# Optimization experiments

Hardware: AMD Instinct MI355X
Metric: run time of the kernel (lower is better)

The kernel has to match this reference:

```python
import jax, jax.numpy as jnp
import numpy as np

IMAGE_SIZE = 128
PATCH_SIZE = 8
BOND_DIM = 128
CP_RANK = 64
EMBED_DIM = 512
BATCH = 512
GRID = IMAGE_SIZE // PATCH_SIZE            # 16
NUM_PATCHES = GRID * GRID                  # 256
DEPTH = 4                                  # log4(256)
LEVEL_NODES = [64, 16, 4, 1]


def setup_inputs() -> dict:
    key = jax.random.key(0)
    ks = jax.random.split(key, 32)
    s = 0.02
    inp = {
        "x": jax.random.normal(ks[0], (BATCH, 1, IMAGE_SIZE, IMAGE_SIZE), jnp.float32),
        "W_patch": jax.random.normal(ks[1], (PATCH_SIZE * PATCH_SIZE, BOND_DIM), jnp.float32) * s,
        "b_patch": jnp.zeros((BOND_DIM,), jnp.float32),
        "pos": jax.random.normal(ks[2], (1, NUM_PATCHES, BOND_DIM), jnp.float32),
        "gamma": jnp.ones((BOND_DIM,), jnp.float32),
        "beta": jnp.zeros((BOND_DIM,), jnp.float32),
        "W_head": jax.random.normal(ks[3], (BOND_DIM, EMBED_DIM), jnp.float32) * s,
        "b_head": jnp.zeros((EMBED_DIM,), jnp.float32),
    }
    for lvl, n in enumerate(LEVEL_NODES):
        # per-node distinct CP factors: 4 children in_dim->rank, then rank->out_dim
        inp[f"f{lvl}"] = jax.random.normal(ks[4 + 2 * lvl], (n, 4, BOND_DIM, CP_RANK), jnp.float32) * s
        inp[f"o{lvl}"] = jax.random.normal(ks[5 + 2 * lvl], (n, CP_RANK, BOND_DIM), jnp.float32) * s
    return inp


def _patchify(x):
    # 'b c (h p1) (w p2) -> b (h w) (p1 p2 c)', c == 1
    b = x.shape[0]
    x = x.reshape(b, 1, GRID, PATCH_SIZE, GRID, PATCH_SIZE)
    x = x.transpose(0, 2, 4, 3, 5, 1)                  # b h w p1 p2 c
    return x.reshape(b, NUM_PATCHES, PATCH_SIZE * PATCH_SIZE)


def _quad_group(x, grid):
    # 'b (h w) c -> b (h/2 w/2) (h2 w2) c' with 2x2 blocks
    b, _, c = x.shape
    g2 = grid // 2
    x = x.reshape(b, g2, 2, g2, 2, c).transpose(0, 1, 3, 2, 4, 5)
    return x.reshape(b, g2 * g2, 4, c)


def _cp_level(x, f, o):
    # x: [b, n, 4, C]; f: [n, 4, C, R]; o: [n, R, C]
    u = jnp.einsum('bnqc,nqcr->bnqr', x, f)
    p = jnp.prod(u, axis=2)                            # [b, n, R]
    return jnp.einsum('bnr,nrc->bnc', p, o)


def reference(x, W_patch, b_patch, pos, f0, o0, f1, o1, f2, o2, f3, o3,
              gamma, beta, W_head, b_head):
    h = _patchify(x) @ W_patch + b_patch               # [b, 256, C]
    h = h + pos
    grid = GRID
    for f, o in ((f0, o0), (f1, o1), (f2, o2), (f3, o3)):
        h = _cp_level(_quad_group(h, grid), f, o)
        grid //= 2
    h = h[:, 0, :]                                     # squeeze node dim
    mu = jnp.mean(h, axis=-1, keepdims=True)
    var = jnp.var(h, axis=-1, keepdims=True)
    h = (h - mu) / jnp.sqrt(var + 1e-5) * gamma + beta
    out = h @ W_head + b_head
    n = jnp.maximum(jnp.linalg.norm(out, axis=-1, keepdims=True), 1e-12)
    return out / n
```

## Files before the change

kernel.cpp:

```cpp
#include <hip/hip_runtime.h>
#include <hip/hip_bf16.h>

#define BATCH     512
#define IMG       128
#define PS        8
#define GRID_P    16
#define NP        256
#define C         128
#define R         64
#define E         512

typedef float f32x4 __attribute__((ext_vector_type(4)));
typedef short s16x8 __attribute__((ext_vector_type(8)));

__device__ __forceinline__ unsigned short f2bf(float x) {
    unsigned int u = __float_as_uint(x);
    u += 0x7fffu + ((u >> 16) & 1u);
    return (unsigned short)(u >> 16);
}
__device__ __forceinline__ float bf2f(unsigned short h) {
    return __uint_as_float(((unsigned int)h) << 16);
}

__global__ __launch_bounds__(256) void prep_all_kernel(
    const float* __restrict__ f0, const float* __restrict__ f1,
    const float* __restrict__ f2, const float* __restrict__ f3,
    const float* __restrict__ o0, const float* __restrict__ o1,
    const float* __restrict__ o2, const float* __restrict__ o3,
    const float* __restrict__ Wh, const float* __restrict__ Wp,
    const float* __restrict__ pos, const float* __restrict__ bp,
    unsigned short* __restrict__ fTL, unsigned short* __restrict__ oT,
    unsigned short* __restrict__ WhT, unsigned short* __restrict__ WfT,
    float* __restrict__ pf)
{
    __shared__ float ls[128 * 68];
    __shared__ float red[64 * 4];
    const int bi = blockIdx.x, t = threadIdx.x;

    if (bi < 256) {
        const float* src = f0 + (size_t)bi * 8192;
#pragma unroll
        for (int i = 0; i < 8; ++i) {
            const int fi = (t + 256 * i) * 4;
            const int c = fi >> 6, r = fi & 63;
            *(float4*)(ls + c * 68 + r) = *(const float4*)(src + fi);
        }
        __syncthreads();

        const int w = t >> 6, lane = t & 63;
        const int m = lane & 15, g = lane >> 4;

        f32x4 acc[4];
#pragma unroll
        for (int nt = 0; nt < 4; ++nt) acc[nt] = (f32x4){0.f, 0.f, 0.f, 0.f};
#pragma unroll
        for (int kt = 0; kt < 4; ++kt) {
            s16x8 afr;
#pragma unroll
            for (int e = 0; e < 8; ++e)
                afr[e] = (short)f2bf(ls[(kt * 32 + g * 8 + e) * 68 + w * 16 + m]);
#pragma unroll
            for (int nt = 0; nt < 4; ++nt) {
                const float* wr = Wp + (size_t)(nt * 16 + m) * 128 + kt * 32 + g * 8;
                const float4 b0 = *(const float4*)wr;
                const float4 b1 = *(const float4*)(wr + 4);
                s16x8 bfr;
                bfr[0] = (short)f2bf(b0.x); bfr[1] = (short)f2bf(b0.y);
                bfr[2] = (short)f2bf(b0.z); bfr[3] = (short)f2bf(b0.w);
                bfr[4] = (short)f2bf(b1.x); bfr[5] = (short)f2bf(b1.y);
                bfr[6] = (short)f2bf(b1.z); bfr[7] = (short)f2bf(b1.w);
                acc[nt] = __builtin_amdgcn_mfma_f32_16x16x32_bf16(afr, bfr, acc[nt], 0, 0, 0);
            }
        }
        unsigned short* D = WfT + (size_t)bi * 4096;
#pragma unroll
        for (int nt = 0; nt < 4; ++nt)
#pragma unroll
            for (int j = 0; j < 4; ++j)
                D[(size_t)(w * 16 + g * 4 + j) * 64 + nt * 16 + m] = f2bf(acc[nt][j]);

        {
            const int r = t & 63, half = t >> 6;
            const int n0 = bi >> 2, q = bi & 3;
            const int pp = (2 * (n0 >> 3) + (q >> 1)) * GRID_P + 2 * (n0 & 7) + (q & 1);
            const float* posr = pos + (size_t)pp * C;
            float s = 0.f;
#pragma unroll 8
            for (int e = 0; e < 32; ++e) {
                const int c = half * 32 + e;
                s += (posr[c] + bp[c]) * ls[c * 68 + r];
            }
            red[r * 4 + half] = s;
        }
        __syncthreads();
        if (t < 64)
            pf[bi * 64 + t] = red[t * 4 + 0] + red[t * 4 + 1] + red[t * 4 + 2] + red[t * 4 + 3];
    } else if (bi < 340) {
        const int ti = bi - 256;
        const float* src;
        if      (ti < 64) src = f1 + (size_t)ti * 8192;
        else if (ti < 80) src = f2 + (size_t)(ti - 64) * 8192;
        else              src = f3 + (size_t)(ti - 80) * 8192;
        unsigned short* dst = fTL + (size_t)ti * 8192;
#pragma unroll
        for (int i = 0; i < 8; ++i) {
            const int fi = (t + 256 * i) * 4;
            const int c = fi >> 6, r = fi & 63;
            *(float4*)(ls + c * 68 + r) = *(const float4*)(src + fi);
        }
        __syncthreads();
        const int rr = t >> 2, seg = t & 3;
        unsigned int* d32 = (unsigned int*)(dst + rr * 128 + seg * 32);
#pragma unroll
        for (int ii = 0; ii < 16; ++ii) {
            const int c = seg * 32 + ii * 2;
            const unsigned int lo = f2bf(ls[c * 68 + rr]);
            const unsigned int hi = f2bf(ls[(c + 1) * 68 + rr]);
            d32[ii] = lo | (hi << 16);
        }
    } else if (bi < 425) {
        const int oi = bi - 340;
        const float* src;
        if      (oi < 64) src = o0 + (size_t)oi * 8192;
        else if (oi < 80) src = o1 + (size_t)(oi - 64) * 8192;
        else if (oi < 84) src = o2 + (size_t)(oi - 80) * 8192;
        else              src = o3 + (size_t)(oi - 84) * 8192;
        unsigned short* dst = oT + (size_t)oi * 8192;
#pragma unroll
        for (int i = 0; i < 8; ++i) {
            const int fi = (t + 256 * i) * 4;
            const int r = fi >> 7, c = fi & 127;
            *(float4*)(ls + r * 132 + c) = *(const float4*)(src + fi);
        }
        __syncthreads();
        const int cc = t >> 1, seg = t & 1;
        unsigned int* d32 = (unsigned int*)(dst + cc * 64 + seg * 32);
#pragma unroll
        for (int ii = 0; ii < 16; ++ii) {
            const int r = seg * 32 + ii * 2;
            const unsigned int lo = f2bf(ls[r * 132 + cc]);
            const unsigned int hi = f2bf(ls[(r + 1) * 132 + cc]);
            d32[ii] = lo | (hi << 16);
        }
    } else {
        const int j = bi - 425;
#pragma unroll
        for (int i = 0; i < 8; ++i) {
            const int fi = (t + 256 * i) * 4;
            const int c = fi >> 6, e = fi & 63;
            *(float4*)(ls + c * 68 + e) = *(const float4*)(Wh + (size_t)c * E + j * 64 + e);
        }
        __syncthreads();
        const int rr = t >> 2, seg = t & 3;
        unsigned int* d32 = (unsigned int*)(WhT + (size_t)(j * 64 + rr) * 128 + seg * 32);
#pragma unroll
        for (int ii = 0; ii < 16; ++ii) {
            const int c = seg * 32 + ii * 2;
            const unsigned int lo = f2bf(ls[c * 68 + rr]);
            const unsigned int hi = f2bf(ls[(c + 1) * 68 + rr]);
            d32[ii] = lo | (hi << 16);
        }
    }
}

__global__ __launch_bounds__(256) void level01_fused(
    const float* __restrict__ x,
    const unsigned short* __restrict__ WfT,
    const float* __restrict__ pf,
    const unsigned short* __restrict__ oT,
    const unsigned short* __restrict__ fT1,
    unsigned short* __restrict__ h2)
{
    __shared__ __align__(16) unsigned short pixs[16 * 1026];
    __shared__ __align__(16) float          us1[4 * 16 * 68];
    __shared__ __align__(16) unsigned short ps0[4 * 16 * 72];
    __shared__ __align__(16) unsigned short ps1[16 * 72];
    __shared__ __align__(16) unsigned short h1s[4 * 16 * 136];

    const int bi = blockIdx.x;
    const int n1 = bi >> 5, btile = bi & 31;
    const int t = threadIdx.x, w = t >> 6, lane = t & 63;
    const int m = lane & 15, g = lane >> 4;
    const int bt = btile * 16;

    const int y1g = n1 >> 2, x1g = n1 & 3;
    const int Ry0 = y1g * 32, Rx0 = x1g * 32;
    const int n0 = (2 * y1g + (w >> 1)) * 8 + 2 * x1g + (w & 1);

#pragma unroll
    for (int i = 0; i < 16; ++i) {
        const int idx = i * 256 + t;
        const int c4 = idx & 7, rowg = (idx >> 3) & 31, bl = idx >> 8;
        const float4 p4 = *(const float4*)(x + ((size_t)(bt + bl) * IMG + Ry0 + rowg) * IMG + Rx0 + c4 * 4);
        uint2 v;
        v.x = (unsigned int)f2bf(p4.x) | ((unsigned int)f2bf(p4.y) << 16);
        v.y = (unsigned int)f2bf(p4.z) | ((unsigned int)f2bf(p4.w) << 16);
        *(uint2*)(pixs + bl * 1026 + rowg * 32 + c4 * 4) = v;
    }
    __syncthreads();

    s16x8 a[4][2];
    {
        const int rbase = 16 * (w >> 1);
        const int cbase = 16 * (w & 1);
#pragma unroll
        for (int q = 0; q < 4; ++q) {
            const int rq = rbase + 8 * (q >> 1) + g;
            const int cc = cbase + 8 * (q & 1);
#pragma unroll
            for (int kt = 0; kt < 2; ++kt)
                a[q][kt] = *(const s16x8*)(pixs + m * 1026 + (rq + kt * 4) * 32 + cc);
        }
    }

    f32x4 accu[4][4];
#pragma unroll
    for (int q = 0; q < 4; ++q) {
        const float* pfq = pf + (size_t)(n0 * 4 + q) * 64;
#pragma unroll
        for (int nt = 0; nt < 4; ++nt) {
            const float pv = pfq[nt * 16 + m];
            accu[q][nt] = (f32x4){pv, pv, pv, pv};
        }
    }
#pragma unroll
    for (int q = 0; q < 4; ++q) {
        const unsigned short* Wq = WfT + (size_t)(n0 * 4 + q) * 4096;
#pragma unroll
        for (int kt = 0; kt < 2; ++kt) {
            const int koff = kt * 32 + g * 8;
#pragma unroll
            for (int nt = 0; nt < 4; ++nt) {
                const s16x8 bfr = *(const s16x8*)(Wq + (size_t)(nt * 16 + m) * 64 + koff);
                accu[q][nt] = __builtin_amdgcn_mfma_f32_16x16x32_bf16(a[q][kt], bfr, accu[q][nt], 0, 0, 0);
            }
        }
    }

    unsigned short* myps = ps0 + w * (16 * 72);
#pragma unroll
    for (int nt = 0; nt < 4; ++nt) {
        const f32x4 pr = accu[0][nt] * accu[1][nt] * accu[2][nt] * accu[3][nt];
#pragma unroll
        for (int j = 0; j < 4; ++j)
            myps[(g * 4 + j) * 72 + nt * 16 + m] = f2bf(pr[j]);
    }

    {
        s16x8 ap[2];
#pragma unroll
        for (int kt = 0; kt < 2; ++kt)
            ap[kt] = *(const s16x8*)(myps + m * 72 + kt * 32 + g * 8);
        const unsigned short* oTn = oT + (size_t)n0 * 8192;
        unsigned short* myh = h1s + w * (16 * 136);
#pragma unroll
        for (int ct = 0; ct < 8; ++ct) {
            f32x4 aco = (f32x4){0.f, 0.f, 0.f, 0.f};
#pragma unroll
            for (int kt = 0; kt < 2; ++kt) {
                const s16x8 bfr = *(const s16x8*)(oTn + (size_t)(ct * 16 + m) * 64 + kt * 32 + g * 8);
                aco = __builtin_amdgcn_mfma_f32_16x16x32_bf16(ap[kt], bfr, aco, 0, 0, 0);
            }
#pragma unroll
            for (int j = 0; j < 4; ++j)
                myh[(g * 4 + j) * 136 + ct * 16 + m] = f2bf(aco[j]);
        }
    }

    {
        const unsigned short* myh = h1s + w * (16 * 136);
        const unsigned short* fq = fT1 + (size_t)(n1 * 4 + w) * 8192;
        f32x4 au[4];
#pragma unroll
        for (int nt = 0; nt < 4; ++nt) au[nt] = (f32x4){0.f, 0.f, 0.f, 0.f};
#pragma unroll
        for (int kt = 0; kt < 4; ++kt) {
            const int koff = kt * 32 + g * 8;
            const s16x8 afr = *(const s16x8*)(myh + m * 136 + koff);
#pragma unroll
            for (int nt = 0; nt < 4; ++nt) {
                const s16x8 bfr = *(const s16x8*)(fq + (size_t)(nt * 16 + m) * 128 + koff);
                au[nt] = __builtin_amdgcn_mfma_f32_16x16x32_bf16(afr, bfr, au[nt], 0, 0, 0);
            }
        }
#pragma unroll
        for (int nt = 0; nt < 4; ++nt)
#pragma unroll
            for (int j = 0; j < 4; ++j)
                us1[(w * 16 + g * 4 + j) * 68 + nt * 16 + m] = au[nt][j];
    }
    __syncthreads();

    {
        const int pb = t >> 4, r0 = (t & 15) * 4;
        const f32x4 u0 = *(const f32x4*)(us1 + (0 * 16 + pb) * 68 + r0);
        const f32x4 u1 = *(const f32x4*)(us1 + (1 * 16 + pb) * 68 + r0);
        const f32x4 u2 = *(const f32x4*)(us1 + (2 * 16 + pb) * 68 + r0);
        const f32x4 u3 = *(const f32x4*)(us1 + (3 * 16 + pb) * 68 + r0);
        const f32x4 p = u0 * u1 * u2 * u3;
        uint2 v;
        v.x = (unsigned int)f2bf(p[0]) | ((unsigned int)f2bf(p[1]) << 16);
        v.y = (unsigned int)f2bf(p[2]) | ((unsigned int)f2bf(p[3]) << 16);
        *(uint2*)(ps1 + pb * 72 + r0) = v;
    }
    __syncthreads();

    {
        s16x8 ap[2];
#pragma unroll
        for (int kt = 0; kt < 2; ++kt)
            ap[kt] = *(const s16x8*)(ps1 + m * 72 + kt * 32 + g * 8);
        const unsigned short* oTn = oT + (size_t)(64 + n1) * 8192;
#pragma unroll
        for (int i = 0; i < 2; ++i) {
            const int ct = w * 2 + i;
            f32x4 aco = (f32x4){0.f, 0.f, 0.f, 0.f};
#pragma unroll
            for (int kt = 0; kt < 2; ++kt) {
                const s16x8 bfr = *(const s16x8*)(oTn + (size_t)(ct * 16 + m) * 64 + kt * 32 + g * 8);
                aco = __builtin_amdgcn_mfma_f32_16x16x32_bf16(ap[kt], bfr, aco, 0, 0, 0);
            }
#pragma unroll
            for (int j = 0; j < 4; ++j)
                h2[((size_t)(bt + g * 4 + j) * 16 + n1) * C + ct * 16 + m] = f2bf(aco[j]);
        }
    }
}

__global__ __launch_bounds__(256) void tail_kernel(
    const unsigned short* __restrict__ h2,
    const unsigned short* __restrict__ fT2,
    const unsigned short* __restrict__ oT2,
    const unsigned short* __restrict__ fT3,
    const unsigned short* __restrict__ oT3,
    const float* __restrict__ gamma, const float* __restrict__ beta,
    const unsigned short* __restrict__ WhT,
    const float* __restrict__ bh,
    float* __restrict__ out)
{
    __shared__ __align__(16) float          us3[4 * 16 * 68];
    __shared__ __align__(16) unsigned short ps2[4 * 16 * 72];
    __shared__ __align__(16) unsigned short ps3[16 * 72];
    __shared__ __align__(16) unsigned short h3s[16 * 4 * 136];
    __shared__ __align__(16) float          h4s[16 * 132];
    __shared__ __align__(16) unsigned short hns[16 * 136];
    __shared__ float red[16 * 4];

    const int bt = blockIdx.x * 16;
    const int t = threadIdx.x, w = t >> 6, lane = t & 63;
    const int m = lane & 15, g = lane >> 4;

    {
        const int n2 = w;
        const int y1 = n2 >> 1, x1 = n2 & 1;
        f32x4 acc_u[4][4];
#pragma unroll
        for (int q = 0; q < 4; ++q)
#pragma unroll
            for (int nt = 0; nt < 4; ++nt) acc_u[q][nt] = (f32x4){0.f, 0.f, 0.f, 0.f};
#pragma unroll
        for (int q = 0; q < 4; ++q) {
            const int pidx = (2 * y1 + (q >> 1)) * 4 + 2 * x1 + (q & 1);
            const unsigned short* xq = h2 + ((size_t)(bt + m) * 16 + pidx) * C;
            const unsigned short* fq = fT2 + (size_t)(n2 * 4 + q) * R * C;
#pragma unroll
            for (int kt = 0; kt < 4; ++kt) {
                const int koff = kt * 32 + g * 8;
                const s16x8 a = *(const s16x8*)(xq + koff);
#pragma unroll
                for (int nt = 0; nt < 4; ++nt) {
                    const s16x8 bfr = *(const s16x8*)(fq + (size_t)(nt * 16 + m) * C + koff);
                    acc_u[q][nt] = __builtin_amdgcn_mfma_f32_16x16x32_bf16(a, bfr, acc_u[q][nt], 0, 0, 0);
                }
            }
        }
        unsigned short* myps = ps2 + w * 16 * 72;
#pragma unroll
        for (int nt = 0; nt < 4; ++nt) {
            const f32x4 p = acc_u[0][nt] * acc_u[1][nt] * acc_u[2][nt] * acc_u[3][nt];
#pragma unroll
            for (int j = 0; j < 4; ++j)
                myps[(g * 4 + j) * 72 + nt * 16 + m] = f2bf(p[j]);
        }
        f32x4 aco[8];
#pragma unroll
        for (int ct = 0; ct < 8; ++ct) aco[ct] = (f32x4){0.f, 0.f, 0.f, 0.f};
        const unsigned short* oTn = oT2 + (size_t)n2 * C * R;
#pragma unroll
        for (int kt = 0; kt < 2; ++kt) {
            const int koff = kt * 32 + g * 8;
            const s16x8 a = *(const s16x8*)(myps + m * 72 + koff);
#pragma unroll
            for (int ct = 0; ct < 8; ++ct) {
                const s16x8 bfr = *(const s16x8*)(oTn + (size_t)(ct * 16 + m) * R + koff);
                aco[ct] = __builtin_amdgcn_mfma_f32_16x16x32_bf16(a, bfr, aco[ct], 0, 0, 0);
            }
        }
#pragma unroll
        for (int ct = 0; ct < 8; ++ct)
#pragma unroll
            for (int j = 0; j < 4; ++j)
                h3s[((g * 4 + j) * 4 + n2) * 136 + ct * 16 + m] = f2bf(aco[ct][j]);
    }
    __syncthreads();

    {
        const int q = w;
        const unsigned short* fq = fT3 + (size_t)q * R * C;
        f32x4 acc_u[4];
#pragma unroll
        for (int nt = 0; nt < 4; ++nt) acc_u[nt] = (f32x4){0.f, 0.f, 0.f, 0.f};
#pragma unroll
        for (int kt = 0; kt < 4; ++kt) {
            const int koff = kt * 32 + g * 8;
            const s16x8 a = *(const s16x8*)(h3s + (m * 4 + q) * 136 + koff);
#pragma unroll
            for (int nt = 0; nt < 4; ++nt) {
                const s16x8 bfr = *(const s16x8*)(fq + (size_t)(nt * 16 + m) * C + koff);
                acc_u[nt] = __builtin_amdgcn_mfma_f32_16x16x32_bf16(a, bfr, acc_u[nt], 0, 0, 0);
            }
        }
#pragma unroll
        for (int nt = 0; nt < 4; ++nt)
#pragma unroll
            for (int j = 0; j < 4; ++j)
                us3[(q * 16 + g * 4 + j) * 68 + nt * 16 + m] = acc_u[nt][j];
    }
    __syncthreads();
    {
        const int pb = t >> 4, r0 = (t & 15) * 4;
        const f32x4 u0 = *(const f32x4*)(us3 + (0 * 16 + pb) * 68 + r0);
        const f32x4 u1 = *(const f32x4*)(us3 + (1 * 16 + pb) * 68 + r0);
        const f32x4 u2 = *(const f32x4*)(us3 + (2 * 16 + pb) * 68 + r0);
        const f32x4 u3 = *(const f32x4*)(us3 + (3 * 16 + pb) * 68 + r0);
        const f32x4 p = u0 * u1 * u2 * u3;
        uint2 v;
        v.x = (unsigned int)f2bf(p[0]) | ((unsigned int)f2bf(p[1]) << 16);
        v.y = (unsigned int)f2bf(p[2]) | ((unsigned int)f2bf(p[3]) << 16);
        *(uint2*)(ps3 + pb * 72 + r0) = v;
    }
    __syncthreads();
    {
        s16x8 ap[2];
#pragma unroll
        for (int kt = 0; kt < 2; ++kt)
            ap[kt] = *(const s16x8*)(ps3 + m * 72 + kt * 32 + g * 8);
#pragma unroll
        for (int i = 0; i < 2; ++i) {
            f32x4 aco = (f32x4){0.f, 0.f, 0.f, 0.f};
            const int ct = w * 2 + i;
#pragma unroll
            for (int kt = 0; kt < 2; ++kt) {
                const s16x8 bfr = *(const s16x8*)(oT3 + (size_t)(ct * 16 + m) * R + kt * 32 + g * 8);
                aco = __builtin_amdgcn_mfma_f32_16x16x32_bf16(ap[kt], bfr, aco, 0, 0, 0);
            }
#pragma unroll
            for (int j = 0; j < 4; ++j)
                h4s[(g * 4 + j) * 132 + ct * 16 + m] = aco[j];
        }
    }
    __syncthreads();

    {
        const int rb = w * 4 + g;
        const int c0 = m * 8;
        const f32x4 v0 = *(const f32x4*)(h4s + rb * 132 + c0);
        const f32x4 v1 = *(const f32x4*)(h4s + rb * 132 + c0 + 4);
        float s  = v0[0] + v0[1] + v0[2] + v0[3] + v1[0] + v1[1] + v1[2] + v1[3];
        float ss = v0[0]*v0[0] + v0[1]*v0[1] + v0[2]*v0[2] + v0[3]*v0[3]
                 + v1[0]*v1[0] + v1[1]*v1[1] + v1[2]*v1[2] + v1[3]*v1[3];
#pragma unroll
        for (int off = 1; off < 16; off <<= 1) {
            s  += __shfl_xor(s, off);
            ss += __shfl_xor(ss, off);
        }
        const float mu   = s * (1.f / C);
        const float var  = ss * (1.f / C) - mu * mu;
        const float rstd = rsqrtf(var + 1e-5f);
        const f32x4 ga0 = *(const f32x4*)(gamma + c0);
        const f32x4 ga1 = *(const f32x4*)(gamma + c0 + 4);
        const f32x4 be0 = *(const f32x4*)(beta + c0);
        const f32x4 be1 = *(const f32x4*)(beta + c0 + 4);
        unsigned int o32[4];
        float hv[8];
#pragma unroll
        for (int k = 0; k < 4; ++k) hv[k]     = (v0[k] - mu) * rstd * ga0[k] + be0[k];
#pragma unroll
        for (int k = 0; k < 4; ++k) hv[4 + k] = (v1[k] - mu) * rstd * ga1[k] + be1[k];
#pragma unroll
        for (int k = 0; k < 4; ++k)
            o32[k] = (unsigned int)f2bf(hv[2*k]) | ((unsigned int)f2bf(hv[2*k+1]) << 16);
        *(uint4*)(hns + rb * 136 + c0) = *(uint4*)o32;
    }
    __syncthreads();

    {
        f32x4 acc[8];
#pragma unroll
        for (int nt = 0; nt < 8; ++nt) {
            const int e = w * 128 + nt * 16 + m;
            const float bv = bh[e];
            acc[nt] = (f32x4){bv, bv, bv, bv};
        }
#pragma unroll
        for (int kt = 0; kt < 4; ++kt) {
            const int koff = kt * 32 + g * 8;
            const s16x8 a = *(const s16x8*)(hns + m * 136 + koff);
#pragma unroll
            for (int nt = 0; nt < 8; ++nt) {
                const int e = w * 128 + nt * 16 + m;
                const s16x8 bfr = *(const s16x8*)(WhT + (size_t)e * 128 + koff);
                acc[nt] = __builtin_amdgcn_mfma_f32_16x16x32_bf16(a, bfr, acc[nt], 0, 0, 0);
            }
        }
        float sq[4];
#pragma unroll
        for (int j = 0; j < 4; ++j) {
            float s = 0.f;
#pragma unroll
            for (int nt = 0; nt < 8; ++nt) s += acc[nt][j] * acc[nt][j];
#pragma unroll
            for (int off = 1; off < 16; off <<= 1) s += __shfl_xor(s, off);
            sq[j] = s;
        }
        if (m == 0) {
#pragma unroll
            for (int j = 0; j < 4; ++j) red[(g * 4 + j) * 4 + w] = sq[j];
        }
        __syncthreads();
#pragma unroll
        for (int j = 0; j < 4; ++j) {
            const int row = g * 4 + j;
            const float tot = red[row * 4 + 0] + red[row * 4 + 1]
                            + red[row * 4 + 2] + red[row * 4 + 3];
            const float inv = 1.f / fmaxf(sqrtf(tot), 1e-12f);
#pragma unroll
            for (int nt = 0; nt < 8; ++nt) {
                const int e = w * 128 + nt * 16 + m;
                out[(size_t)(bt + row) * E + e] = acc[nt][j] * inv;
            }
        }
    }
}

extern "C" void kernel_launch(void* const* d_in, const int* in_sizes, int n_in,
                              void* d_out, int out_size, void* d_ws, size_t ws_size,
                              hipStream_t stream) {
    const float* x     = (const float*)d_in[0];
    const float* Wp    = (const float*)d_in[1];
    const float* bp    = (const float*)d_in[2];
    const float* pos   = (const float*)d_in[3];
    const float* gamma = (const float*)d_in[4];
    const float* beta  = (const float*)d_in[5];
    const float* Wh    = (const float*)d_in[6];
    const float* bh    = (const float*)d_in[7];
    const float* f0    = (const float*)d_in[8];
    const float* o0    = (const float*)d_in[9];
    const float* f1    = (const float*)d_in[10];
    const float* o1    = (const float*)d_in[11];
    const float* f2    = (const float*)d_in[12];
    const float* o2    = (const float*)d_in[13];
    const float* f3    = (const float*)d_in[14];
    const float* o3    = (const float*)d_in[15];
    float* out = (float*)d_out;

    unsigned short* h2  = (unsigned short*)d_ws;
    unsigned short* fTL = h2 + (size_t)1048576;
    unsigned short* oT  = fTL + (size_t)688128;
    unsigned short* WfT = oT + (size_t)696320;
    unsigned short* WhT = WfT + (size_t)1048576;
    float*          pff = (float*)(WhT + 65536);

    unsigned short* fT1 = fTL;
    unsigned short* fT2 = fTL + (size_t)64 * 8192;
    unsigned short* fT3 = fTL + (size_t)80 * 8192;
    unsigned short* oT2 = oT + (size_t)80 * 8192;
    unsigned short* oT3 = oT + (size_t)84 * 8192;

    prep_all_kernel<<<433, 256, 0, stream>>>(f0, f1, f2, f3, o0, o1, o2, o3,
                                             Wh, Wp, pos, bp,
                                             fTL, oT, WhT, WfT, pff);

    level01_fused<<<16 * 32, 256, 0, stream>>>(x, WfT, pff, oT, fT1, h2);

    tail_kernel<<<32, 256, 0, stream>>>(h2, fT2, oT2, fT3, oT3,
                                        gamma, beta, WhT, bh, out);
}
```

Baseline: 152.5 us.

## Fuse prep, level01 and tail kernels into one cooperative mega-kernel

```diff
diff --git a/kernel.cpp b/kernel.cpp
--- a/kernel.cpp
+++ b/kernel.cpp
@@ -1,5 +1,8 @@
 #include <hip/hip_runtime.h>
 #include <hip/hip_bf16.h>
+#include <hip/hip_cooperative_groups.h>
+
+namespace cg = cooperative_groups;
 
 #define BATCH     512
 #define IMG       128
@@ -22,522 +25,514 @@
     return __uint_as_float(((unsigned int)h) << 16);
 }
 
-__global__ __launch_bounds__(256) void prep_all_kernel(
-    const float* __restrict__ f0, const float* __restrict__ f1,
-    const float* __restrict__ f2, const float* __restrict__ f3,
-    const float* __restrict__ o0, const float* __restrict__ o1,
-    const float* __restrict__ o2, const float* __restrict__ o3,
-    const float* __restrict__ Wh, const float* __restrict__ Wp,
-    const float* __restrict__ pos, const float* __restrict__ bp,
+__global__ __launch_bounds__(256) void ttn_mega_kernel(
+    const float* __restrict__ x,  const float* __restrict__ Wp,
+    const float* __restrict__ bp, const float* __restrict__ pos,
+    const float* __restrict__ gamma, const float* __restrict__ beta,
+    const float* __restrict__ Wh, const float* __restrict__ bh,
+    const float* __restrict__ f0, const float* __restrict__ o0,
+    const float* __restrict__ f1, const float* __restrict__ o1,
+    const float* __restrict__ f2, const float* __restrict__ o2,
+    const float* __restrict__ f3, const float* __restrict__ o3,
     unsigned short* __restrict__ fTL, unsigned short* __restrict__ oT,
     unsigned short* __restrict__ WhT, unsigned short* __restrict__ WfT,
-    float* __restrict__ pf)
-{
-    __shared__ float ls[128 * 68];
-    __shared__ float red[64 * 4];
-    const int bi = blockIdx.x, t = threadIdx.x;
-
-    if (bi < 256) {
-        const float* src = f0 + (size_t)bi * 8192;
-#pragma unroll
-        for (int i = 0; i < 8; ++i) {
-            const int fi = (t + 256 * i) * 4;
-            const int c = fi >> 6, r = fi & 63;
-            *(float4*)(ls + c * 68 + r) = *(const float4*)(src + fi);
-        }
-        __syncthreads();
-
-        const int w = t >> 6, lane = t & 63;
-        const int m = lane & 15, g = lane >> 4;
-
-        f32x4 acc[4];
-#pragma unroll
-        for (int nt = 0; nt < 4; ++nt) acc[nt] = (f32x4){0.f, 0.f, 0.f, 0.f};
-#pragma unroll
-        for (int kt = 0; kt < 4; ++kt) {
-            s16x8 afr;
-#pragma unroll
-            for (int e = 0; e < 8; ++e)
-                afr[e] = (short)f2bf(ls[(kt * 32 + g * 8 + e) * 68 + w * 16 + m]);
-#pragma unroll
-            for (int nt = 0; nt < 4; ++nt) {
-                const float* wr = Wp + (size_t)(nt * 16 + m) * 128 + kt * 32 + g * 8;
-                const float4 b0 = *(const float4*)wr;
-                const float4 b1 = *(const float4*)(wr + 4);
-                s16x8 bfr;
-                bfr[0] = (short)f2bf(b0.x); bfr[1] = (short)f2bf(b0.y);
-                bfr[2] = (short)f2bf(b0.z); bfr[3] = (short)f2bf(b0.w);
-                bfr[4] = (short)f2bf(b1.x); bfr[5] = (short)f2bf(b1.y);
-                bfr[6] = (short)f2bf(b1.z); bfr[7] = (short)f2bf(b1.w);
-                acc[nt] = __builtin_amdgcn_mfma_f32_16x16x32_bf16(afr, bfr, acc[nt], 0, 0, 0);
-            }
-        }
-        unsigned short* D = WfT + (size_t)bi * 4096;
-#pragma unroll
-        for (int nt = 0; nt < 4; ++nt)
-#pragma unroll
-            for (int j = 0; j < 4; ++j)
-                D[(size_t)(w * 16 + g * 4 + j) * 64 + nt * 16 + m] = f2bf(acc[nt][j]);
-
-        {
-            const int r = t & 63, half = t >> 6;
-            const int n0 = bi >> 2, q = bi & 3;
-            const int pp = (2 * (n0 >> 3) + (q >> 1)) * GRID_P + 2 * (n0 & 7) + (q & 1);
-            const float* posr = pos + (size_t)pp * C;
-            float s = 0.f;
-#pragma unroll 8
-            for (int e = 0; e < 32; ++e) {
-                const int c = half * 32 + e;
-                s += (posr[c] + bp[c]) * ls[c * 68 + r];
-            }
-            red[r * 4 + half] = s;
-        }
-        __syncthreads();
-        if (t < 64)
-            pf[bi * 64 + t] = red[t * 4 + 0] + red[t * 4 + 1] + red[t * 4 + 2] + red[t * 4 + 3];
-    } else if (bi < 340) {
-        const int ti = bi - 256;
-        const float* src;
-        if      (ti < 64) src = f1 + (size_t)ti * 8192;
-        else if (ti < 80) src = f2 + (size_t)(ti - 64) * 8192;
-        else              src = f3 + (size_t)(ti - 80) * 8192;
-        unsigned short* dst = fTL + (size_t)ti * 8192;
-#pragma unroll
-        for (int i = 0; i < 8; ++i) {
-            const int fi = (t + 256 * i) * 4;
-            const int c = fi >> 6, r = fi & 63;
-            *(float4*)(ls + c * 68 + r) = *(const float4*)(src + fi);
-        }
-        __syncthreads();
-        const int rr = t >> 2, seg = t & 3;
-        unsigned int* d32 = (unsigned int*)(dst + rr * 128 + seg * 32);
-#pragma unroll
-        for (int ii = 0; ii < 16; ++ii) {
-            const int c = seg * 32 + ii * 2;
-            const unsigned int lo = f2bf(ls[c * 68 + rr]);
-            const unsigned int hi = f2bf(ls[(c + 1) * 68 + rr]);
-            d32[ii] = lo | (hi << 16);
-        }
-    } else if (bi < 425) {
-        const int oi = bi - 340;
-        const float* src;
-        if      (oi < 64) src = o0 + (size_t)oi * 8192;
-        else if (oi < 80) src = o1 + (size_t)(oi - 64) * 8192;
-        else if (oi < 84) src = o2 + (size_t)(oi - 80) * 8192;
-        else              src = o3 + (size_t)(oi - 84) * 8192;
-        unsigned short* dst = oT + (size_t)oi * 8192;
-#pragma unroll
-        for (int i = 0; i < 8; ++i) {
-            const int fi = (t + 256 * i) * 4;
-            const int r = fi >> 7, c = fi & 127;
-            *(float4*)(ls + r * 132 + c) = *(const float4*)(src + fi);
-        }
-        __syncthreads();
-        const int cc = t >> 1, seg = t & 1;
-        unsigned int* d32 = (unsigned int*)(dst + cc * 64 + seg * 32);
-#pragma unroll
-        for (int ii = 0; ii < 16; ++ii) {
-            const int r = seg * 32 + ii * 2;
-            const unsigned int lo = f2bf(ls[r * 132 + cc]);
-            const unsigned int hi = f2bf(ls[(r + 1) * 132 + cc]);
-            d32[ii] = lo | (hi << 16);
-        }
-    } else {
-        const int j = bi - 425;
-#pragma unroll
-        for (int i = 0; i < 8; ++i) {
-            const int fi = (t + 256 * i) * 4;
-            const int c = fi >> 6, e = fi & 63;
-            *(float4*)(ls + c * 68 + e) = *(const float4*)(Wh + (size_t)c * E + j * 64 + e);
-        }
-        __syncthreads();
-        const int rr = t >> 2, seg = t & 3;
-        unsigned int* d32 = (unsigned int*)(WhT + (size_t)(j * 64 + rr) * 128 + seg * 32);
-#pragma unroll
-        for (int ii = 0; ii < 16; ++ii) {
-            const int c = seg * 32 + ii * 2;
-            const unsigned int lo = f2bf(ls[c * 68 + rr]);
-            const unsigned int hi = f2bf(ls[(c + 1) * 68 + rr]);
-            d32[ii] = lo | (hi << 16);
-        }
-    }
-}
-
-__global__ __launch_bounds__(256) void level01_fused(
-    const float* __restrict__ x,
-    const unsigned short* __restrict__ WfT,
-    const float* __restrict__ pf,
-    const unsigned short* __restrict__ oT,
-    const unsigned short* __restrict__ fT1,
-    unsigned short* __restrict__ h2)
-{
-    __shared__ __align__(16) unsigned short pixs[16 * 1026];
-    __shared__ __align__(16) float          us1[4 * 16 * 68];
-    __shared__ __align__(16) unsigned short ps0[4 * 16 * 72];
-    __shared__ __align__(16) unsigned short ps1[16 * 72];
-    __shared__ __align__(16) unsigned short h1s[4 * 16 * 136];
-
-    const int bi = blockIdx.x;
-    const int n1 = bi >> 5, btile = bi & 31;
-    const int t = threadIdx.x, w = t >> 6, lane = t & 63;
-    const int m = lane & 15, g = lane >> 4;
-    const int bt = btile * 16;
-
-    const int y1g = n1 >> 2, x1g = n1 & 3;
-    const int Ry0 = y1g * 32, Rx0 = x1g * 32;
-    const int n0 = (2 * y1g + (w >> 1)) * 8 + 2 * x1g + (w & 1);
-
-#pragma unroll
-    for (int i = 0; i < 16; ++i) {
-        const int idx = i * 256 + t;
-        const int c4 = idx & 7, rowg = (idx >> 3) & 31, bl = idx >> 8;
-        const float4 p4 = *(const float4*)(x + ((size_t)(bt + bl) * IMG + Ry0 + rowg) * IMG + Rx0 + c4 * 4);
-        uint2 v;
-        v.x = (unsigned int)f2bf(p4.x) | ((unsigned int)f2bf(p4.y) << 16);
-        v.y = (unsigned int)f2bf(p4.z) | ((unsigned int)f2bf(p4.w) << 16);
-        *(uint2*)(pixs + bl * 1026 + rowg * 32 + c4 * 4) = v;
-    }
-    __syncthreads();
-
-    s16x8 a[4][2];
-    {
-        const int rbase = 16 * (w >> 1);
-        const int cbase = 16 * (w & 1);
-#pragma unroll
-        for (int q = 0; q < 4; ++q) {
-            const int rq = rbase + 8 * (q >> 1) + g;
-            const int cc = cbase + 8 * (q & 1);
-#pragma unroll
-            for (int kt = 0; kt < 2; ++kt)
-                a[q][kt] = *(const s16x8*)(pixs + m * 1026 + (rq + kt * 4) * 32 + cc);
-        }
-    }
-
-    f32x4 accu[4][4];
-#pragma unroll
-    for (int q = 0; q < 4; ++q) {
-        const float* pfq = pf + (size_t)(n0 * 4 + q) * 64;
-#pragma unroll
-        for (int nt = 0; nt < 4; ++nt) {
-            const float pv = pfq[nt * 16 + m];
-            accu[q][nt] = (f32x4){pv, pv, pv, pv};
-        }
-    }
-#pragma unroll
-    for (int q = 0; q < 4; ++q) {
-        const unsigned short* Wq = WfT + (size_t)(n0 * 4 + q) * 4096;
-#pragma unroll
-        for (int kt = 0; kt < 2; ++kt) {
-            const int koff = kt * 32 + g * 8;
-#pragma unroll
-            for (int nt = 0; nt < 4; ++nt) {
-                const s16x8 bfr = *(const s16x8*)(Wq + (size_t)(nt * 16 + m) * 64 + koff);
-                accu[q][nt] = __builtin_amdgcn_mfma_f32_16x16x32_bf16(a[q][kt], bfr, accu[q][nt], 0, 0, 0);
-            }
-        }
-    }
-
-    unsigned short* myps = ps0 + w * (16 * 72);
-#pragma unroll
-    for (int nt = 0; nt < 4; ++nt) {
-        const f32x4 pr = accu[0][nt] * accu[1][nt] * accu[2][nt] * accu[3][nt];
-#pragma unroll
-        for (int j = 0; j < 4; ++j)
-            myps[(g * 4 + j) * 72 + nt * 16 + m] = f2bf(pr[j]);
-    }
-
-    {
-        s16x8 ap[2];
-#pragma unroll
-        for (int kt = 0; kt < 2; ++kt)
-            ap[kt] = *(const s16x8*)(myps + m * 72 + kt * 32 + g * 8);
-        const unsigned short* oTn = oT + (size_t)n0 * 8192;
-        unsigned short* myh = h1s + w * (16 * 136);
-#pragma unroll
-        for (int ct = 0; ct < 8; ++ct) {
-            f32x4 aco = (f32x4){0.f, 0.f, 0.f, 0.f};
-#pragma unroll
-            for (int kt = 0; kt < 2; ++kt) {
-                const s16x8 bfr = *(const s16x8*)(oTn + (size_t)(ct * 16 + m) * 64 + kt * 32 + g * 8);
-                aco = __builtin_amdgcn_mfma_f32_16x16x32_bf16(ap[kt], bfr, aco, 0, 0, 0);
-            }
-#pragma unroll
-            for (int j = 0; j < 4; ++j)
-                myh[(g * 4 + j) * 136 + ct * 16 + m] = f2bf(aco[j]);
-        }
-    }
-
-    {
-        const unsigned short* myh = h1s + w * (16 * 136);
-        const unsigned short* fq = fT1 + (size_t)(n1 * 4 + w) * 8192;
-        f32x4 au[4];
-#pragma unroll
-        for (int nt = 0; nt < 4; ++nt) au[nt] = (f32x4){0.f, 0.f, 0.f, 0.f};
-#pragma unroll
-        for (int kt = 0; kt < 4; ++kt) {
-            const int koff = kt * 32 + g * 8;
-            const s16x8 afr = *(const s16x8*)(myh + m * 136 + koff);
-#pragma unroll
-            for (int nt = 0; nt < 4; ++nt) {
-                const s16x8 bfr = *(const s16x8*)(fq + (size_t)(nt * 16 + m) * 128 + koff);
-                au[nt] = __builtin_amdgcn_mfma_f32_16x16x32_bf16(afr, bfr, au[nt], 0, 0, 0);
-            }
-        }
-#pragma unroll
-        for (int nt = 0; nt < 4; ++nt)
-#pragma unroll
-            for (int j = 0; j < 4; ++j)
-                us1[(w * 16 + g * 4 + j) * 68 + nt * 16 + m] = au[nt][j];
-    }
-    __syncthreads();
-
-    {
-        const int pb = t >> 4, r0 = (t & 15) * 4;
-        const f32x4 u0 = *(const f32x4*)(us1 + (0 * 16 + pb) * 68 + r0);
-        const f32x4 u1 = *(const f32x4*)(us1 + (1 * 16 + pb) * 68 + r0);
-        const f32x4 u2 = *(const f32x4*)(us1 + (2 * 16 + pb) * 68 + r0);
-        const f32x4 u3 = *(const f32x4*)(us1 + (3 * 16 + pb) * 68 + r0);
-        const f32x4 p = u0 * u1 * u2 * u3;
-        uint2 v;
-        v.x = (unsigned int)f2bf(p[0]) | ((unsigned int)f2bf(p[1]) << 16);
-        v.y = (unsigned int)f2bf(p[2]) | ((unsigned int)f2bf(p[3]) << 16);
-        *(uint2*)(ps1 + pb * 72 + r0) = v;
-    }
-    __syncthreads();
-
-    {
-        s16x8 ap[2];
-#pragma unroll
-        for (int kt = 0; kt < 2; ++kt)
-            ap[kt] = *(const s16x8*)(ps1 + m * 72 + kt * 32 + g * 8);
-        const unsigned short* oTn = oT + (size_t)(64 + n1) * 8192;
-#pragma unroll
-        for (int i = 0; i < 2; ++i) {
-            const int ct = w * 2 + i;
-            f32x4 aco = (f32x4){0.f, 0.f, 0.f, 0.f};
-#pragma unroll
-            for (int kt = 0; kt < 2; ++kt) {
-                const s16x8 bfr = *(const s16x8*)(oTn + (size_t)(ct * 16 + m) * 64 + kt * 32 + g * 8);
-                aco = __builtin_amdgcn_mfma_f32_16x16x32_bf16(ap[kt], bfr, aco, 0, 0, 0);
-            }
-#pragma unroll
-            for (int j = 0; j < 4; ++j)
-                h2[((size_t)(bt + g * 4 + j) * 16 + n1) * C + ct * 16 + m] = f2bf(aco[j]);
-        }
-    }
-}
-
-__global__ __launch_bounds__(256) void tail_kernel(
-    const unsigned short* __restrict__ h2,
-    const unsigned short* __restrict__ fT2,
-    const unsigned short* __restrict__ oT2,
-    const unsigned short* __restrict__ fT3,
-    const unsigned short* __restrict__ oT3,
-    const float* __restrict__ gamma, const float* __restrict__ beta,
-    const unsigned short* __restrict__ WhT,
-    const float* __restrict__ bh,
+    float* __restrict__ pf, unsigned short* __restrict__ h2,
     float* __restrict__ out)
 {
-    __shared__ __align__(16) float          us3[4 * 16 * 68];
-    __shared__ __align__(16) unsigned short ps2[4 * 16 * 72];
-    __shared__ __align__(16) unsigned short ps3[16 * 72];
-    __shared__ __align__(16) unsigned short h3s[16 * 4 * 136];
-    __shared__ __align__(16) float          h4s[16 * 132];
-    __shared__ __align__(16) unsigned short hns[16 * 136];
-    __shared__ float red[16 * 4];
-
-    const int bt = blockIdx.x * 16;
-    const int t = threadIdx.x, w = t >> 6, lane = t & 63;
+    __shared__ __align__(16) char smem[46336];
+    cg::grid_group grid = cg::this_grid();
+
+    const int bi = blockIdx.x, t = threadIdx.x;
+    const int w = t >> 6, lane = t & 63;
     const int m = lane & 15, g = lane >> 4;
 
+    if (bi < 433) {
+        float* ls  = (float*)smem;
+        float* red = (float*)(smem + 34816);
+
+        if (bi < 256) {
+            const float* src = f0 + (size_t)bi * 8192;
+#pragma unroll
+            for (int i = 0; i < 8; ++i) {
+                const int fi = (t + 256 * i) * 4;
+                const int c = fi >> 6, r = fi & 63;
+                *(float4*)(ls + c * 68 + r) = *(const float4*)(src + fi);
+            }
+            __syncthreads();
+
+            f32x4 acc[4];
+#pragma unroll
+            for (int nt = 0; nt < 4; ++nt) acc[nt] = (f32x4){0.f, 0.f, 0.f, 0.f};
+#pragma unroll
+            for (int kt = 0; kt < 4; ++kt) {
+                s16x8 afr;
+#pragma unroll
+                for (int e = 0; e < 8; ++e)
+                    afr[e] = (short)f2bf(ls[(kt * 32 + g * 8 + e) * 68 + w * 16 + m]);
+#pragma unroll
+                for (int nt = 0; nt < 4; ++nt) {
+                    const float* wr = Wp + (size_t)(nt * 16 + m) * 128 + kt * 32 + g * 8;
+                    const float4 b0 = *(const float4*)wr;
+                    const float4 b1 = *(const float4*)(wr + 4);
+                    s16x8 bfr;
+                    bfr[0] = (short)f2bf(b0.x); bfr[1] = (short)f2bf(b0.y);
+                    bfr[2] = (short)f2bf(b0.z); bfr[3] = (short)f2bf(b0.w);
+                    bfr[4] = (short)f2bf(b1.x); bfr[5] = (short)f2bf(b1.y);
+                    bfr[6] = (short)f2bf(b1.z); bfr[7] = (short)f2bf(b1.w);
+                    acc[nt] = __builtin_amdgcn_mfma_f32_16x16x32_bf16(afr, bfr, acc[nt], 0, 0, 0);
+                }
+            }
+            unsigned short* D = WfT + (size_t)bi * 4096;
+#pragma unroll
+            for (int nt = 0; nt < 4; ++nt)
+#pragma unroll
+                for (int j = 0; j < 4; ++j)
+                    D[(size_t)(w * 16 + g * 4 + j) * 64 + nt * 16 + m] = f2bf(acc[nt][j]);
+
+            {
+                const int r = t & 63, half = t >> 6;
+                const int n0 = bi >> 2, q = bi & 3;
+                const int pp = (2 * (n0 >> 3) + (q >> 1)) * GRID_P + 2 * (n0 & 7) + (q & 1);
+                const float* posr = pos + (size_t)pp * C;
+                float s = 0.f;
+#pragma unroll 8
+                for (int e = 0; e < 32; ++e) {
+                    const int c = half * 32 + e;
+                    s += (posr[c] + bp[c]) * ls[c * 68 + r];
+                }
+                red[r * 4 + half] = s;
+            }
+            __syncthreads();
+            if (t < 64)
+                pf[bi * 64 + t] = red[t * 4 + 0] + red[t * 4 + 1] + red[t * 4 + 2] + red[t * 4 + 3];
+        } else if (bi < 340) {
+            const int ti = bi - 256;
+            const float* src;
+            if      (ti < 64) src = f1 + (size_t)ti * 8192;
+            else if (ti < 80) src = f2 + (size_t)(ti - 64) * 8192;
+            else              src = f3 + (size_t)(ti - 80) * 8192;
+            unsigned short* dst = fTL + (size_t)ti * 8192;
+#pragma unroll
+            for (int i = 0; i < 8; ++i) {
+                const int fi = (t + 256 * i) * 4;
+                const int c = fi >> 6, r = fi & 63;
+                *(float4*)(ls + c * 68 + r) = *(const float4*)(src + fi);
+            }
+            __syncthreads();
+            const int rr = t >> 2, seg = t & 3;
+            unsigned int* d32 = (unsigned int*)(dst + rr * 128 + seg * 32);
+#pragma unroll
+            for (int ii = 0; ii < 16; ++ii) {
+                const int c = seg * 32 + ii * 2;
+                const unsigned int lo = f2bf(ls[c * 68 + rr]);
+                const unsigned int hi = f2bf(ls[(c + 1) * 68 + rr]);
+                d32[ii] = lo | (hi << 16);
+            }
+        } else if (bi < 425) {
+            const int oi = bi - 340;
+            const float* src;
+            if      (oi < 64) src = o0 + (size_t)oi * 8192;
+            else if (oi < 80) src = o1 + (size_t)(oi - 64) * 8192;
+            else if (oi < 84) src = o2 + (size_t)(oi - 80) * 8192;
+            else              src = o3 + (size_t)(oi - 84) * 8192;
+            unsigned short* dst = oT + (size_t)oi * 8192;
+#pragma unroll
+            for (int i = 0; i < 8; ++i) {
+                const int fi = (t + 256 * i) * 4;
+                const int r = fi >> 7, c = fi & 127;
+                *(float4*)(ls + r * 132 + c) = *(const float4*)(src + fi);
+            }
+            __syncthreads();
+            const int cc = t >> 1, seg = t & 1;
+            unsigned int* d32 = (unsigned int*)(dst + cc * 64 + seg * 32);
+#pragma unroll
+            for (int ii = 0; ii < 16; ++ii) {
+                const int r = seg * 32 + ii * 2;
+                const unsigned int lo = f2bf(ls[r * 132 + cc]);
+                const unsigned int hi = f2bf(ls[(r + 1) * 132 + cc]);
+                d32[ii] = lo | (hi << 16);
+            }
+        } else {
+            const int j = bi - 425;
+#pragma unroll
+            for (int i = 0; i < 8; ++i) {
+                const int fi = (t + 256 * i) * 4;
+                const int c = fi >> 6, e = fi & 63;
+                *(float4*)(ls + c * 68 + e) = *(const float4*)(Wh + (size_t)c * E + j * 64 + e);
+            }
+            __syncthreads();
+            const int rr = t >> 2, seg = t & 3;
+            unsigned int* d32 = (unsigned int*)(WhT + (size_t)(j * 64 + rr) * 128 + seg * 32);
+#pragma unroll
+            for (int ii = 0; ii < 16; ++ii) {
+                const int c = seg * 32 + ii * 2;
+                const unsigned int lo = f2bf(ls[c * 68 + rr]);
+                const unsigned int hi = f2bf(ls[(c + 1) * 68 + rr]);
+                d32[ii] = lo | (hi << 16);
+            }
+        }
+    }
+    grid.sync();
+
     {
-        const int n2 = w;
-        const int y1 = n2 >> 1, x1 = n2 & 1;
-        f32x4 acc_u[4][4];
-#pragma unroll
-        for (int q = 0; q < 4; ++q)
-#pragma unroll
-            for (int nt = 0; nt < 4; ++nt) acc_u[q][nt] = (f32x4){0.f, 0.f, 0.f, 0.f};
+        unsigned short* pixs = (unsigned short*)smem;
+        float*          us1  = (float*)smem;
+        unsigned short* ps0  = (unsigned short*)(smem + 17408);
+        unsigned short* ps1  = (unsigned short*)(smem + 26624);
+        unsigned short* h1s  = (unsigned short*)(smem + 28928);
+
+        const int n1 = bi >> 5, btile = bi & 31;
+        const int bt = btile * 16;
+        const int y1g = n1 >> 2, x1g = n1 & 3;
+        const int Ry0 = y1g * 32, Rx0 = x1g * 32;
+        const int n0 = (2 * y1g + (w >> 1)) * 8 + 2 * x1g + (w & 1);
+
+#pragma unroll
+        for (int i = 0; i < 16; ++i) {
+            const int idx = i * 256 + t;
+            const int c4 = idx & 7, rowg = (idx >> 3) & 31, bl = idx >> 8;
+            const float4 p4 = *(const float4*)(x + ((size_t)(bt + bl) * IMG + Ry0 + rowg) * IMG + Rx0 + c4 * 4);
+            uint2 v;
+            v.x = (unsigned int)f2bf(p4.x) | ((unsigned int)f2bf(p4.y) << 16);
+            v.y = (unsigned int)f2bf(p4.z) | ((unsigned int)f2bf(p4.w) << 16);
+            *(uint2*)(pixs + bl * 1026 + rowg * 32 + c4 * 4) = v;
+        }
+        __syncthreads();
+
+        s16x8 a[4][2];
+        {
+            const int rbase = 16 * (w >> 1);
+            const int cbase = 16 * (w & 1);
+#pragma unroll
+            for (int q = 0; q < 4; ++q) {
+                const int rq = rbase + 8 * (q >> 1) + g;
+                const int cc = cbase + 8 * (q & 1);
+#pragma unroll
+                for (int kt = 0; kt < 2; ++kt)
+                    a[q][kt] = *(const s16x8*)(pixs + m * 1026 + (rq + kt * 4) * 32 + cc);
+            }
+        }
+        __syncthreads();
+
+        f32x4 accu[4][4];
 #pragma unroll
         for (int q = 0; q < 4; ++q) {
-            const int pidx = (2 * y1 + (q >> 1)) * 4 + 2 * x1 + (q & 1);
-            const unsigned short* xq = h2 + ((size_t)(bt + m) * 16 + pidx) * C;
-            const unsigned short* fq = fT2 + (size_t)(n2 * 4 + q) * R * C;
+            const float* pfq = pf + (size_t)(n0 * 4 + q) * 64;
+#pragma unroll
+            for (int nt = 0; nt < 4; ++nt) {
+                const float pv = pfq[nt * 16 + m];
+                accu[q][nt] = (f32x4){pv, pv, pv, pv};
+            }
+        }
+#pragma unroll
+        for (int q = 0; q < 4; ++q) {
+            const unsigned short* Wq = WfT + (size_t)(n0 * 4 + q) * 4096;
+#pragma unroll
+            for (int kt = 0; kt < 2; ++kt) {
+                const int koff = kt * 32 + g * 8;
+#pragma unroll
+                for (int nt = 0; nt < 4; ++nt) {
+                    const s16x8 bfr = *(const s16x8*)(Wq + (size_t)(nt * 16 + m) * 64 + koff);
+                    accu[q][nt] = __builtin_amdgcn_mfma_f32_16x16x32_bf16(a[q][kt], bfr, accu[q][nt], 0, 0, 0);
+                }
+            }
+        }
+
+        unsigned short* myps = ps0 + w * (16 * 72);
+#pragma unroll
+        for (int nt = 0; nt < 4; ++nt) {
+            const f32x4 pr = accu[0][nt] * accu[1][nt] * accu[2][nt] * accu[3][nt];
+#pragma unroll
+            for (int j = 0; j < 4; ++j)
+                myps[(g * 4 + j) * 72 + nt * 16 + m] = f2bf(pr[j]);
+        }
+
+        {
+            s16x8 ap[2];
+#pragma unroll
+            for (int kt = 0; kt < 2; ++kt)
+                ap[kt] = *(const s16x8*)(myps + m * 72 + kt * 32 + g * 8);
+            const unsigned short* oTn = oT + (size_t)n0 * 8192;
+            unsigned short* myh = h1s + w * (16 * 136);
+#pragma unroll
+            for (int ct = 0; ct < 8; ++ct) {
+                f32x4 aco = (f32x4){0.f, 0.f, 0.f, 0.f};
+#pragma unroll
+                for (int kt = 0; kt < 2; ++kt) {
+                    const s16x8 bfr = *(const s16x8*)(oTn + (size_t)(ct * 16 + m) * 64 + kt * 32 + g * 8);
+                    aco = __builtin_amdgcn_mfma_f32_16x16x32_bf16(ap[kt], bfr, aco, 0, 0, 0);
+                }
+#pragma unroll
+                for (int j = 0; j < 4; ++j)
+                    myh[(g * 4 + j) * 136 + ct * 16 + m] = f2bf(aco[j]);
+            }
+        }
+
+        {
+            const unsigned short* myh = h1s + w * (16 * 136);
+            const unsigned short* fq = fTL + (size_t)(n1 * 4 + w) * 8192;
+            f32x4 au[4];
+#pragma unroll
+            for (int nt = 0; nt < 4; ++nt) au[nt] = (f32x4){0.f, 0.f, 0.f, 0.f};
 #pragma unroll
             for (int kt = 0; kt < 4; ++kt) {
                 const int koff = kt * 32 + g * 8;
-                const s16x8 a = *(const s16x8*)(xq + koff);
+                const s16x8 afr = *(const s16x8*)(myh + m * 136 + koff);
+#pragma unroll
+                for (int nt = 0; nt < 4; ++nt) {
+                    const s16x8 bfr = *(const s16x8*)(fq + (size_t)(nt * 16 + m) * 128 + koff);
+                    au[nt] = __builtin_amdgcn_mfma_f32_16x16x32_bf16(afr, bfr, au[nt], 0, 0, 0);
+                }
+            }
+#pragma unroll
+            for (int nt = 0; nt < 4; ++nt)
+#pragma unroll
+                for (int j = 0; j < 4; ++j)
+                    us1[(w * 16 + g * 4 + j) * 68 + nt * 16 + m] = au[nt][j];
+        }
+        __syncthreads();
+
+        {
+            const int pb = t >> 4, r0 = (t & 15) * 4;
+            const f32x4 u0 = *(const f32x4*)(us1 + (0 * 16 + pb) * 68 + r0);
+            const f32x4 u1 = *(const f32x4*)(us1 + (1 * 16 + pb) * 68 + r0);
+            const f32x4 u2 = *(const f32x4*)(us1 + (2 * 16 + pb) * 68 + r0);
+            const f32x4 u3 = *(const f32x4*)(us1 + (3 * 16 + pb) * 68 + r0);
+            const f32x4 p = u0 * u1 * u2 * u3;
+            uint2 v;
+            v.x = (unsigned int)f2bf(p[0]) | ((unsigned int)f2bf(p[1]) << 16);
+            v.y = (unsigned int)f2bf(p[2]) | ((unsigned int)f2bf(p[3]) << 16);
+            *(uint2*)(ps1 + pb * 72 + r0) = v;
+        }
+        __syncthreads();
+
+        {
+            s16x8 ap[2];
+#pragma unroll
+            for (int kt = 0; kt < 2; ++kt)
+                ap[kt] = *(const s16x8*)(ps1 + m * 72 + kt * 32 + g * 8);
+            const unsigned short* oTn = oT + (size_t)(64 + n1) * 8192;
+#pragma unroll
+            for (int i = 0; i < 2; ++i) {
+                const int ct = w * 2 + i;
+                f32x4 aco = (f32x4){0.f, 0.f, 0.f, 0.f};
+#pragma unroll
+                for (int kt = 0; kt < 2; ++kt) {
+                    const s16x8 bfr = *(const s16x8*)(oTn + (size_t)(ct * 16 + m) * 64 + kt * 32 + g * 8);
+                    aco = __builtin_amdgcn_mfma_f32_16x16x32_bf16(ap[kt], bfr, aco, 0, 0, 0);
+                }
+#pragma unroll
+                for (int j = 0; j < 4; ++j)
+                    h2[((size_t)(bt + g * 4 + j) * 16 + n1) * C + ct * 16 + m] = f2bf(aco[j]);
+            }
+        }
+    }
+    grid.sync();
+
+    if (bi < 32) {
+        float*          us3 = (float*)smem;
+        float*          h4s = (float*)smem;
+        unsigned short* hns = (unsigned short*)(smem + 8448);
+        float*          red = (float*)(smem + 12800);
+        unsigned short* ps2 = (unsigned short*)(smem + 17408);
+        unsigned short* ps3 = (unsigned short*)(smem + 26624);
+        unsigned short* h3s = (unsigned short*)(smem + 28928);
+
+        const int bt = bi * 16;
+        const unsigned short* fT2 = fTL + (size_t)64 * 8192;
+        const unsigned short* fT3 = fTL + (size_t)80 * 8192;
+        const unsigned short* oT2 = oT + (size_t)80 * 8192;
+        const unsigned short* oT3 = oT + (size_t)84 * 8192;
+
+        {
+            const int n2 = w;
+            const int y1 = n2 >> 1, x1 = n2 & 1;
+            f32x4 acc_u[4][4];
+#pragma unroll
+            for (int q = 0; q < 4; ++q)
+#pragma unroll
+                for (int nt = 0; nt < 4; ++nt) acc_u[q][nt] = (f32x4){0.f, 0.f, 0.f, 0.f};
+#pragma unroll
+            for (int q = 0; q < 4; ++q) {
+                const int pidx = (2 * y1 + (q >> 1)) * 4 + 2 * x1 + (q & 1);
+                const unsigned short* xq = h2 + ((size_t)(bt + m) * 16 + pidx) * C;
+                const unsigned short* fq = fT2 + (size_t)(n2 * 4 + q) * R * C;
+#pragma unroll
+                for (int kt = 0; kt < 4; ++kt) {
+                    const int koff = kt * 32 + g * 8;
+                    const s16x8 afr = *(const s16x8*)(xq + koff);
+#pragma unroll
+                    for (int nt = 0; nt < 4; ++nt) {
+                        const s16x8 bfr = *(const s16x8*)(fq + (size_t)(nt * 16 + m) * C + koff);
+                        acc_u[q][nt] = __builtin_amdgcn_mfma_f32_16x16x32_bf16(afr, bfr, acc_u[q][nt], 0, 0, 0);
+                    }
+                }
+            }
+            unsigned short* myps = ps2 + w * 16 * 72;
+#pragma unroll
+            for (int nt = 0; nt < 4; ++nt) {
+                const f32x4 p = acc_u[0][nt] * acc_u[1][nt] * acc_u[2][nt] * acc_u[3][nt];
+#pragma unroll
+                for (int j = 0; j < 4; ++j)
+                    myps[(g * 4 + j) * 72 + nt * 16 + m] = f2bf(p[j]);
+            }
+            f32x4 aco[8];
+#pragma unroll
+            for (int ct = 0; ct < 8; ++ct) aco[ct] = (f32x4){0.f, 0.f, 0.f, 0.f};
+            const unsigned short* oTn = oT2 + (size_t)n2 * C * R;
+#pragma unroll
+            for (int kt = 0; kt < 2; ++kt) {
+                const int koff = kt * 32 + g * 8;
+                const s16x8 afr = *(const s16x8*)(myps + m * 72 + koff);
+#pragma unroll
+                for (int ct = 0; ct < 8; ++ct) {
+                    const s16x8 bfr = *(const s16x8*)(oTn + (size_t)(ct * 16 + m) * R + koff);
+                    aco[ct] = __builtin_amdgcn_mfma_f32_16x16x32_bf16(afr, bfr, aco[ct], 0, 0, 0);
+                }
+            }
+#pragma unroll
+            for (int ct = 0; ct < 8; ++ct)
+#pragma unroll
+                for (int j = 0; j < 4; ++j)
+                    h3s[((g * 4 + j) * 4 + n2) * 136 + ct * 16 + m] = f2bf(aco[ct][j]);
+        }
+        __syncthreads();
+
+        {
+            const int q = w;
+            const unsigned short* fq = fT3 + (size_t)q * R * C;
+            f32x4 acc_u[4];
+#pragma unroll
+            for (int nt = 0; nt < 4; ++nt) acc_u[nt] = (f32x4){0.f, 0.f, 0.f, 0.f};
+#pragma unroll
+            for (int kt = 0; kt < 4; ++kt) {
+                const int koff = kt * 32 + g * 8;
+                const s16x8 afr = *(const s16x8*)(h3s + (m * 4 + q) * 136 + koff);
 #pragma unroll
                 for (int nt = 0; nt < 4; ++nt) {
                     const s16x8 bfr = *(const s16x8*)(fq + (size_t)(nt * 16 + m) * C + koff);
-                    acc_u[q][nt] = __builtin_amdgcn_mfma_f32_16x16x32_bf16(a, bfr, acc_u[q][nt], 0, 0, 0);
-                }
-            }
-        }
-        unsigned short* myps = ps2 + w * 16 * 72;
-#pragma unroll
-        for (int nt = 0; nt < 4; ++nt) {
-            const f32x4 p = acc_u[0][nt] * acc_u[1][nt] * acc_u[2][nt] * acc_u[3][nt];
-#pragma unroll
-            for (int j = 0; j < 4; ++j)
-                myps[(g * 4 + j) * 72 + nt * 16 + m] = f2bf(p[j]);
-        }
-        f32x4 aco[8];
-#pragma unroll
-        for (int ct = 0; ct < 8; ++ct) aco[ct] = (f32x4){0.f, 0.f, 0.f, 0.f};
-        const unsigned short* oTn = oT2 + (size_t)n2 * C * R;
-#pragma unroll
-        for (int kt = 0; kt < 2; ++kt) {
-            const int koff = kt * 32 + g * 8;
-            const s16x8 a = *(const s16x8*)(myps + m * 72 + koff);
-#pragma unroll
-            for (int ct = 0; ct < 8; ++ct) {
-                const s16x8 bfr = *(const s16x8*)(oTn + (size_t)(ct * 16 + m) * R + koff);
-                aco[ct] = __builtin_amdgcn_mfma_f32_16x16x32_bf16(a, bfr, aco[ct], 0, 0, 0);
-            }
-        }
-#pragma unroll
-        for (int ct = 0; ct < 8; ++ct)
-#pragma unroll
-            for (int j = 0; j < 4; ++j)
-                h3s[((g * 4 + j) * 4 + n2) * 136 + ct * 16 + m] = f2bf(aco[ct][j]);
-    }
-    __syncthreads();
-
-    {
-        const int q = w;
-        const unsigned short* fq = fT3 + (size_t)q * R * C;
-        f32x4 acc_u[4];
-#pragma unroll
-        for (int nt = 0; nt < 4; ++nt) acc_u[nt] = (f32x4){0.f, 0.f, 0.f, 0.f};
-#pragma unroll
-        for (int kt = 0; kt < 4; ++kt) {
-            const int koff = kt * 32 + g * 8;
-            const s16x8 a = *(const s16x8*)(h3s + (m * 4 + q) * 136 + koff);
-#pragma unroll
-            for (int nt = 0; nt < 4; ++nt) {
-                const s16x8 bfr = *(const s16x8*)(fq + (size_t)(nt * 16 + m) * C + koff);
-                acc_u[nt] = __builtin_amdgcn_mfma_f32_16x16x32_bf16(a, bfr, acc_u[nt], 0, 0, 0);
-            }
-        }
-#pragma unroll
-        for (int nt = 0; nt < 4; ++nt)
-#pragma unroll
-            for (int j = 0; j < 4; ++j)
-                us3[(q * 16 + g * 4 + j) * 68 + nt * 16 + m] = acc_u[nt][j];
-    }
-    __syncthreads();
-    {
-        const int pb = t >> 4, r0 = (t & 15) * 4;
-        const f32x4 u0 = *(const f32x4*)(us3 + (0 * 16 + pb) * 68 + r0);
-        const f32x4 u1 = *(const f32x4*)(us3 + (1 * 16 + pb) * 68 + r0);
-        const f32x4 u2 = *(const f32x4*)(us3 + (2 * 16 + pb) * 68 + r0);
-        const f32x4 u3 = *(const f32x4*)(us3 + (3 * 16 + pb) * 68 + r0);
-        const f32x4 p = u0 * u1 * u2 * u3;
-        uint2 v;
-        v.x = (unsigned int)f2bf(p[0]) | ((unsigned int)f2bf(p[1]) << 16);
-        v.y = (unsigned int)f2bf(p[2]) | ((unsigned int)f2bf(p[3]) << 16);
-        *(uint2*)(ps3 + pb * 72 + r0) = v;
-    }
-    __syncthreads();
-    {
-        s16x8 ap[2];
-#pragma unroll
-        for (int kt = 0; kt < 2; ++kt)
-            ap[kt] = *(const s16x8*)(ps3 + m * 72 + kt * 32 + g * 8);
-#pragma unroll
-        for (int i = 0; i < 2; ++i) {
-            f32x4 aco = (f32x4){0.f, 0.f, 0.f, 0.f};
-            const int ct = w * 2 + i;
-#pragma unroll
-            for (int kt = 0; kt < 2; ++kt) {
-                const s16x8 bfr = *(const s16x8*)(oT3 + (size_t)(ct * 16 + m) * R + kt * 32 + g * 8);
-                aco = __builtin_amdgcn_mfma_f32_16x16x32_bf16(ap[kt], bfr, aco, 0, 0, 0);
-            }
-#pragma unroll
-            for (int j = 0; j < 4; ++j)
-                h4s[(g * 4 + j) * 132 + ct * 16 + m] = aco[j];
-        }
-    }
-    __syncthreads();
-
-    {
-        const int rb = w * 4 + g;
-        const int c0 = m * 8;
-        const f32x4 v0 = *(const f32x4*)(h4s + rb * 132 + c0);
-        const f32x4 v1 = *(const f32x4*)(h4s + rb * 132 + c0 + 4);
-        float s  = v0[0] + v0[1] + v0[2] + v0[3] + v1[0] + v1[1] + v1[2] + v1[3];
-        float ss = v0[0]*v0[0] + v0[1]*v0[1] + v0[2]*v0[2] + v0[3]*v0[3]
-                 + v1[0]*v1[0] + v1[1]*v1[1] + v1[2]*v1[2] + v1[3]*v1[3];
-#pragma unroll
-        for (int off = 1; off < 16; off <<= 1) {
-            s  += __shfl_xor(s, off);
-            ss += __shfl_xor(ss, off);
-        }
-        const float mu   = s * (1.f / C);
-        const float var  = ss * (1.f / C) - mu * mu;
-        const float rstd = rsqrtf(var + 1e-5f);
-        const f32x4 ga0 = *(const f32x4*)(gamma + c0);
-        const f32x4 ga1 = *(const f32x4*)(gamma + c0 + 4);
-        const f32x4 be0 = *(const f32x4*)(beta + c0);
-        const f32x4 be1 = *(const f32x4*)(beta + c0 + 4);
-        unsigned int o32[4];
-        float hv[8];
-#pragma unroll
-        for (int k = 0; k < 4; ++k) hv[k]     = (v0[k] - mu) * rstd * ga0[k] + be0[k];
-#pragma unroll
-        for (int k = 0; k < 4; ++k) hv[4 + k] = (v1[k] - mu) * rstd * ga1[k] + be1[k];
-#pragma unroll
-        for (int k = 0; k < 4; ++k)
-            o32[k] = (unsigned int)f2bf(hv[2*k]) | ((unsigned int)f2bf(hv[2*k+1]) << 16);
-        *(uint4*)(hns + rb * 136 + c0) = *(uint4*)o32;
-    }
-    __syncthreads();
-
-    {
-        f32x4 acc[8];
-#pragma unroll
-        for (int nt = 0; nt < 8; ++nt) {
-            const int e = w * 128 + nt * 16 + m;
-            const float bv = bh[e];
-            acc[nt] = (f32x4){bv, bv, bv, bv};
-        }
-#pragma unroll
-        for (int kt = 0; kt < 4; ++kt) {
-            const int koff = kt * 32 + g * 8;
-            const s16x8 a = *(const s16x8*)(hns + m * 136 + koff);
+                    acc_u[nt] = __builtin_amdgcn_mfma_f32_16x16x32_bf16(afr, bfr, acc_u[nt], 0, 0, 0);
+                }
+            }
+#pragma unroll
+            for (int nt = 0; nt < 4; ++nt)
+#pragma unroll
+                for (int j = 0; j < 4; ++j)
+                    us3[(q * 16 + g * 4 + j) * 68 + nt * 16 + m] = acc_u[nt][j];
+        }
+        __syncthreads();
+        {
+            const int pb = t >> 4, r0 = (t & 15) * 4;
+            const f32x4 u0 = *(const f32x4*)(us3 + (0 * 16 + pb) * 68 + r0);
+            const f32x4 u1 = *(const f32x4*)(us3 + (1 * 16 + pb) * 68 + r0);
+            const f32x4 u2 = *(const f32x4*)(us3 + (2 * 16 + pb) * 68 + r0);
+            const f32x4 u3 = *(const f32x4*)(us3 + (3 * 16 + pb) * 68 + r0);
+            const f32x4 p = u0 * u1 * u2 * u3;
+            uint2 v;
+            v.x = (unsigned int)f2bf(p[0]) | ((unsigned int)f2bf(p[1]) << 16);
+            v.y = (unsigned int)f2bf(p[2]) | ((unsigned int)f2bf(p[3]) << 16);
+            *(uint2*)(ps3 + pb * 72 + r0) = v;
+        }
+        __syncthreads();
+        {
+            s16x8 ap[2];
+#pragma unroll
+            for (int kt = 0; kt < 2; ++kt)
+                ap[kt] = *(const s16x8*)(ps3 + m * 72 + kt * 32 + g * 8);
+#pragma unroll
+            for (int i = 0; i < 2; ++i) {
+                f32x4 aco = (f32x4){0.f, 0.f, 0.f, 0.f};
+                const int ct = w * 2 + i;
+#pragma unroll
+                for (int kt = 0; kt < 2; ++kt) {
+                    const s16x8 bfr = *(const s16x8*)(oT3 + (size_t)(ct * 16 + m) * R + kt * 32 + g * 8);
+                    aco = __builtin_amdgcn_mfma_f32_16x16x32_bf16(ap[kt], bfr, aco, 0, 0, 0);
+                }
+#pragma unroll
+                for (int j = 0; j < 4; ++j)
+                    h4s[(g * 4 + j) * 132 + ct * 16 + m] = aco[j];
+            }
+        }
+        __syncthreads();
+
+        {
+            const int rb = w * 4 + g;
+            const int c0 = m * 8;
+            const f32x4 v0 = *(const f32x4*)(h4s + rb * 132 + c0);
+            const f32x4 v1 = *(const f32x4*)(h4s + rb * 132 + c0 + 4);
+            float s  = v0[0] + v0[1] + v0[2] + v0[3] + v1[0] + v1[1] + v1[2] + v1[3];
+            float ss = v0[0]*v0[0] + v0[1]*v0[1] + v0[2]*v0[2] + v0[3]*v0[3]
+                     + v1[0]*v1[0] + v1[1]*v1[1] + v1[2]*v1[2] + v1[3]*v1[3];
+#pragma unroll
+            for (int off = 1; off < 16; off <<= 1) {
+                s  += __shfl_xor(s, off);
+                ss += __shfl_xor(ss, off);
+            }
+            const float mu   = s * (1.f / C);
+            const float var  = ss * (1.f / C) - mu * mu;
+            const float rstd = rsqrtf(var + 1e-5f);
+            const f32x4 ga0 = *(const f32x4*)(gamma + c0);
+            const f32x4 ga1 = *(const f32x4*)(gamma + c0 + 4);
+            const f32x4 be0 = *(const f32x4*)(beta + c0);
+            const f32x4 be1 = *(const f32x4*)(beta + c0 + 4);
+            unsigned int o32[4];
+            float hv[8];
+#pragma unroll
+            for (int k = 0; k < 4; ++k) hv[k]     = (v0[k] - mu) * rstd * ga0[k] + be0[k];
+#pragma unroll
+            for (int k = 0; k < 4; ++k) hv[4 + k] = (v1[k] - mu) * rstd * ga1[k] + be1[k];
+#pragma unroll
+            for (int k = 0; k < 4; ++k)
+                o32[k] = (unsigned int)f2bf(hv[2*k]) | ((unsigned int)f2bf(hv[2*k+1]) << 16);
+            *(uint4*)(hns + rb * 136 + c0) = *(uint4*)o32;
+        }
+        __syncthreads();
+
+        {
+            f32x4 acc[8];
 #pragma unroll
             for (int nt = 0; nt < 8; ++nt) {
                 const int e = w * 128 + nt * 16 + m;
-                const s16x8 bfr = *(const s16x8*)(WhT + (size_t)e * 128 + koff);
-                acc[nt] = __builtin_amdgcn_mfma_f32_16x16x32_bf16(a, bfr, acc[nt], 0, 0, 0);
-            }
-        }
-        float sq[4];
-#pragma unroll
-        for (int j = 0; j < 4; ++j) {
-            float s = 0.f;
-#pragma unroll
-            for (int nt = 0; nt < 8; ++nt) s += acc[nt][j] * acc[nt][j];
-#pragma unroll
-            for (int off = 1; off < 16; off <<= 1) s += __shfl_xor(s, off);
-            sq[j] = s;
-        }
-        if (m == 0) {
-#pragma unroll
-            for (int j = 0; j < 4; ++j) red[(g * 4 + j) * 4 + w] = sq[j];
-        }
-        __syncthreads();
-#pragma unroll
-        for (int j = 0; j < 4; ++j) {
-            const int row = g * 4 + j;
-            const float tot = red[row * 4 + 0] + red[row * 4 + 1]
-                            + red[row * 4 + 2] + red[row * 4 + 3];
-            const float inv = 1.f / fmaxf(sqrtf(tot), 1e-12f);
-#pragma unroll
-            for (int nt = 0; nt < 8; ++nt) {
-                const int e = w * 128 + nt * 16 + m;
-                out[(size_t)(bt + row) * E + e] = acc[nt][j] * inv;
+                const float bv = bh[e];
+                acc[nt] = (f32x4){bv, bv, bv, bv};
+            }
+#pragma unroll
+            for (int kt = 0; kt < 4; ++kt) {
+                const int koff = kt * 32 + g * 8;
+                const s16x8 afr = *(const s16x8*)(hns + m * 136 + koff);
+#pragma unroll
+                for (int nt = 0; nt < 8; ++nt) {
+                    const int e = w * 128 + nt * 16 + m;
+                    const s16x8 bfr = *(const s16x8*)(WhT + (size_t)e * 128 + koff);
+                    acc[nt] = __builtin_amdgcn_mfma_f32_16x16x32_bf16(afr, bfr, acc[nt], 0, 0, 0);
+                }
+            }
+            float sq[4];
+#pragma unroll
+            for (int j = 0; j < 4; ++j) {
+                float s = 0.f;
+#pragma unroll
+                for (int nt = 0; nt < 8; ++nt) s += acc[nt][j] * acc[nt][j];
+#pragma unroll
+                for (int off = 1; off < 16; off <<= 1) s += __shfl_xor(s, off);
+                sq[j] = s;
+            }
+            if (m == 0) {
+#pragma unroll
+                for (int j = 0; j < 4; ++j) red[(g * 4 + j) * 4 + w] = sq[j];
+            }
+            __syncthreads();
+#pragma unroll
+            for (int j = 0; j < 4; ++j) {
+                const int row = g * 4 + j;
+                const float tot = red[row * 4 + 0] + red[row * 4 + 1]
+                                + red[row * 4 + 2] + red[row * 4 + 3];
+                const float inv = 1.f / fmaxf(sqrtf(tot), 1e-12f);
+#pragma unroll
+                for (int nt = 0; nt < 8; ++nt) {
+                    const int e = w * 128 + nt * 16 + m;
+                    out[(size_t)(bt + row) * E + e] = acc[nt][j] * inv;
+                }
             }
         }
     }
@@ -571,18 +566,14 @@
     unsigned short* WhT = WfT + (size_t)1048576;
     float*          pff = (float*)(WhT + 65536);
 
-    unsigned short* fT1 = fTL;
-    unsigned short* fT2 = fTL + (size_t)64 * 8192;
-    unsigned short* fT3 = fTL + (size_t)80 * 8192;
-    unsigned short* oT2 = oT + (size_t)80 * 8192;
-    unsigned short* oT3 = oT + (size_t)84 * 8192;
-
-    prep_all_kernel<<<433, 256, 0, stream>>>(f0, f1, f2, f3, o0, o1, o2, o3,
-                                             Wh, Wp, pos, bp,
-                                             fTL, oT, WhT, WfT, pff);
-
-    level01_fused<<<16 * 32, 256, 0, stream>>>(x, WfT, pff, oT, fT1, h2);
-
-    tail_kernel<<<32, 256, 0, stream>>>(h2, fT2, oT2, fT3, oT3,
-                                        gamma, beta, WhT, bh, out);
+    void* args[] = {
+        (void*)&x, (void*)&Wp, (void*)&bp, (void*)&pos,
+        (void*)&gamma, (void*)&beta, (void*)&Wh, (void*)&bh,
+        (void*)&f0, (void*)&o0, (void*)&f1, (void*)&o1,
+        (void*)&f2, (void*)&o2, (void*)&f3, (void*)&o3,
+        (void*)&fTL, (void*)&oT, (void*)&WhT, (void*)&WfT,
+        (void*)&pff, (void*)&h2, (void*)&out
+    };
+    hipLaunchCooperativeKernel((void*)ttn_mega_kernel, dim3(512), dim3(256),
+                               args, 0, stream);
 }
```

After: 309.0 us. +102.6%, slower.
